# Performance work log

Hardware: AMD Instinct MI355X
Metric: run time of the kernel (lower is better)

## Reference

```python
import jax, jax.numpy as jnp
import numpy as np

NUM_HEADS = 16
D_MODEL = 1024
HEAD_DIM = D_MODEL // NUM_HEADS
SCALE = 8.0 / HEAD_DIM  # use_mup=True
LN_EPS = 1e-5


def setup_inputs() -> dict:
    key = jax.random.key(0)
    ks = jax.random.split(key, 8)
    B, N, M = 2, 2048, 2048
    std = 1.0 / np.sqrt(D_MODEL)
    return {
        "x1": jax.random.normal(ks[0], (B, N, D_MODEL), jnp.float32),
        "x2": jax.random.normal(ks[1], (B, M, D_MODEL), jnp.float32),
        "Wq": jax.random.normal(ks[2], (D_MODEL, D_MODEL), jnp.float32) * std,
        "Wk": jax.random.normal(ks[3], (D_MODEL, D_MODEL), jnp.float32) * std,
        "Wv": jax.random.normal(ks[4], (D_MODEL, D_MODEL), jnp.float32) * std,
        "Wp": jax.random.normal(ks[5], (D_MODEL, D_MODEL), jnp.float32) * std,
        "bp": jnp.zeros((D_MODEL,), jnp.float32),
        "ln_g": jnp.ones((HEAD_DIM,), jnp.float32),
        "ln_b": jnp.zeros((HEAD_DIM,), jnp.float32),
    }


def _layernorm(x, g, b):
    # LayerNorm over last dim (head_dim), eps=1e-5, biased variance (torch default)
    mu = jnp.mean(x, axis=-1, keepdims=True)
    var = jnp.mean(jnp.square(x - mu), axis=-1, keepdims=True)
    return (x - mu) * jax.lax.rsqrt(var + LN_EPS) * g + b


def reference(x1, x2, Wq, Wk, Wv, Wp, bp, ln_g, ln_b):
    B, N, C = x1.shape
    M = x2.shape[1]
    H, D = NUM_HEADS, HEAD_DIM
    # torch Linear: y = x @ W.T  (no qkv bias); reshape to [B, H, L, D]
    q = (x1 @ Wq.T).reshape(B, N, H, D).transpose(0, 2, 1, 3)
    k = (x2 @ Wk.T).reshape(B, M, H, D).transpose(0, 2, 1, 3)
    v = (x2 @ Wv.T).reshape(B, M, H, D).transpose(0, 2, 1, 3)
    # per-head QK LayerNorm (shared params)
    q = _layernorm(q, ln_g, ln_b)
    k = _layernorm(k, ln_g, ln_b)
    q = q * SCALE
    attn = jnp.einsum("bhnd,bhmd->bhnm", q, k)
    attn = jax.nn.softmax(attn, axis=-1)  # causal=False, attn_drop=0
    out = jnp.einsum("bhnm,bhmd->bhnd", attn, v)
    out = out.transpose(0, 2, 1, 3).reshape(B, N, C)
    return out @ Wp.T + bp
```

## Files before the change

kernel.cpp:

```cpp
#include <hip/hip_runtime.h>

#define DEV static __device__ __forceinline__

using bf16x8 = __attribute__((ext_vector_type(8))) short;
using f32x4  = __attribute__((ext_vector_type(4))) float;
using f32x16 = __attribute__((ext_vector_type(16))) float;

#if __has_builtin(__builtin_amdgcn_exp2f)
#define EXP2(x) __builtin_amdgcn_exp2f(x)
#else
#define EXP2(x) exp2f(x)
#endif

DEV unsigned short f2bf(float f) {
  union { float f; unsigned u; } v; v.f = f;
  return (unsigned short)((v.u + 0x7fffu + ((v.u >> 16) & 1u)) >> 16);
}
DEV float bf2f(unsigned short b) {
  union { unsigned u; float f; } v; v.u = ((unsigned)b) << 16;
  return v.f;
}
DEV unsigned cvtpk(float lo, float hi) {
  unsigned r;
  asm("v_cvt_pk_bf16_f32 %0, %1, %2" : "=v"(r) : "v"(lo), "v"(hi));
  return r;
}
DEV void pl32swap(unsigned &a, unsigned &b) {
  asm("v_permlane32_swap_b32 %0, %1" : "+v"(a), "+v"(b));
}
DEV bf16x8 mk8(unsigned a, unsigned b, unsigned c, unsigned d) {
  union { unsigned u[4]; bf16x8 v; } t;
  t.u[0] = a; t.u[1] = b; t.u[2] = c; t.u[3] = d;
  return t.v;
}
DEV f32x4 mfma16(bf16x8 a, bf16x8 b, f32x4 c) {
  return __builtin_amdgcn_mfma_f32_16x16x32_bf16(a, b, c, 0, 0, 0);
}
DEV f32x16 mfma32(bf16x8 a, bf16x8 b, f32x16 c) {
  return __builtin_amdgcn_mfma_f32_32x32x16_bf16(a, b, c, 0, 0, 0);
}
DEV f32x16 zero16() {
  f32x16 z;
#pragma unroll
  for (int i = 0; i < 16; ++i) z[i] = 0.f;
  return z;
}

typedef const __attribute__((address_space(1))) unsigned int* gas1;
typedef __attribute__((address_space(3))) unsigned int* las3;
DEV void gl16(const void* g, void* l) {
  __builtin_amdgcn_global_load_lds((gas1)g, (las3)l, 16, 0, 0);
}

__global__ __launch_bounds__(256, 8)
void conv_bf16(const float* __restrict__ x1, const float* __restrict__ x2,
               const float* __restrict__ Wq, const float* __restrict__ Wk,
               const float* __restrict__ Wv, const float* __restrict__ Wp,
               unsigned short* __restrict__ o)
{
  size_t e = ((size_t)blockIdx.x * 256 + threadIdx.x) * 8;
  const float* s; size_t off;
  if (e < 4194304u)       { s = x1; off = e; }
  else if (e < 8388608u)  { s = x2; off = e - 4194304u; }
  else if (e < 9437184u)  { s = Wq; off = e - 8388608u; }
  else if (e < 10485760u) { s = Wk; off = e - 9437184u; }
  else if (e < 11534336u) { s = Wv; off = e - 10485760u; }
  else                    { s = Wp; off = e - 11534336u; }
  const float4* p = reinterpret_cast<const float4*>(s + off);
  float4 a = p[0], b = p[1];
  int4 r;
  r.x = (int)cvtpk(a.x, a.y); r.y = (int)cvtpk(a.z, a.w);
  r.z = (int)cvtpk(b.x, b.y); r.w = (int)cvtpk(b.z, b.w);
  *reinterpret_cast<int4*>(o + e) = r;
}

__global__ __launch_bounds__(256, 2)
void gemm_qkv_bf(const unsigned short* __restrict__ xb,
                 const float* __restrict__ lg, const float* __restrict__ lb,
                 unsigned short* __restrict__ qb, unsigned short* __restrict__ kb,
                 unsigned short* __restrict__ vtb)
{
  __shared__ short As[128 * 64];
  __shared__ short Bs[128 * 64];
  const int tid = threadIdx.x;
  const int l = tid & 63, w = tid >> 6;
  const int wr = w >> 1, wc = w & 1;
  const int z = blockIdx.z;
  const unsigned short* A = (z == 0) ? xb : (xb + 4194304);
  const unsigned short* W = xb + 8388608 + (size_t)z * 1048576;
  const int id = blockIdx.x + (blockIdx.y << 3);
  const int tl = ((id & 7) << 5) | (id >> 3);
  const int bx = tl & 7, by = tl >> 3;
  const int brow = by * 128, bcol = bx * 128;

  const f32x4 zero = {0.f, 0.f, 0.f, 0.f};
  f32x4 acc[4][4];
#pragma unroll
  for (int mi = 0; mi < 4; ++mi)
#pragma unroll
    for (int ni = 0; ni < 4; ++ni) acc[mi][ni] = zero;

  const int srow = w * 32 + (l >> 3);
  const int scol = (l & 7) * 8;

  for (int kt = 0; kt < 16; ++kt) {
    const unsigned short* ga = A + (size_t)(brow + srow) * 1024 + kt * 64 + scol;
    const unsigned short* gb = W + (size_t)(bcol + srow) * 1024 + kt * 64 + scol;
#pragma unroll
    for (int i = 0; i < 4; ++i) {
      gl16(ga + (size_t)i * 8 * 1024, &As[(w * 32 + i * 8) * 64]);
      gl16(gb + (size_t)i * 8 * 1024, &Bs[(w * 32 + i * 8) * 64]);
    }
    __syncthreads();
#pragma unroll
    for (int kk = 0; kk < 2; ++kk) {
      const int k0 = kk * 32 + ((l >> 4) << 3);
      bf16x8 af[4], bfr[4];
#pragma unroll
      for (int mi = 0; mi < 4; ++mi)
        af[mi] = *reinterpret_cast<const bf16x8*>(
            &As[((wr << 6) + (mi << 4) + (l & 15)) * 64 + k0]);
#pragma unroll
      for (int ni = 0; ni < 4; ++ni)
        bfr[ni] = *reinterpret_cast<const bf16x8*>(
            &Bs[((wc << 6) + (ni << 4) + (l & 15)) * 64 + k0]);
#pragma unroll
      for (int mi = 0; mi < 4; ++mi)
#pragma unroll
        for (int ni = 0; ni < 4; ++ni)
          acc[mi][ni] = mfma16(af[mi], bfr[ni], acc[mi][ni]);
    }
    __syncthreads();
  }

  if (z < 2) {
    unsigned short* dst = (z == 0) ? qb : kb;
    const float scl = (z == 0) ? 0.18033688011112042f : 1.0f;
    const int h = bx * 2 + wc;
    float gw4[4], bw4[4];
#pragma unroll
    for (int ni = 0; ni < 4; ++ni) {
      gw4[ni] = lg[ni * 16 + (l & 15)] * scl;
      bw4[ni] = lb[ni * 16 + (l & 15)] * scl;
    }
#pragma unroll
    for (int mi = 0; mi < 4; ++mi) {
      float ylo[4];
#pragma unroll
      for (int r = 0; r < 4; ++r) {
        float v0 = acc[mi][0][r], v1 = acc[mi][1][r];
        float v2 = acc[mi][2][r], v3 = acc[mi][3][r];
        float s  = (v0 + v1) + (v2 + v3);
        float s2 = (v0 * v0 + v1 * v1) + (v2 * v2 + v3 * v3);
#pragma unroll
        for (int off = 1; off < 16; off <<= 1) {
          s  += __shfl_xor(s, off);
          s2 += __shfl_xor(s2, off);
        }
        float mean = s * (1.f / 64.f);
        float var  = s2 * (1.f / 64.f) - mean * mean;
        float rstd = rsqrtf(var + 1e-5f);
        float y[4];
        y[0] = (v0 - mean) * rstd * gw4[0] + bw4[0];
        y[1] = (v1 - mean) * rstd * gw4[1] + bw4[1];
        y[2] = (v2 - mean) * rstd * gw4[2] + bw4[2];
        y[3] = (v3 - mean) * rstd * gw4[3] + bw4[3];
        if (!(r & 1)) {
          ylo[0] = y[0]; ylo[1] = y[1]; ylo[2] = y[2]; ylo[3] = y[3];
        } else {
          int rowg0 = brow + (wr << 6) + (mi << 4) + ((l >> 4) << 2) + r - 1;
          int b = rowg0 >> 11, n = rowg0 & 2047;
          unsigned short* base =
              dst + (((size_t)(b * 16 + h) << 11) + n) * 64 + (l & 15);
#pragma unroll
          for (int ni = 0; ni < 4; ++ni) {
            unsigned u = cvtpk(ylo[ni], y[ni]);
            base[ni * 16]      = (unsigned short)(u & 0xffffu);
            base[ni * 16 + 64] = (unsigned short)(u >> 16);
          }
        }
      }
    }
  } else {
    const int bb = brow >> 11;
    const int nblk = brow & 2047;
#pragma unroll
    for (int mi = 0; mi < 4; ++mi)
#pragma unroll
      for (int ni = 0; ni < 4; ++ni) {
        int n0 = nblk + (wr << 6) + (mi << 4) + ((l >> 4) << 2);
        int colg = bcol + (wc << 6) + (ni << 4) + (l & 15);
        int h = colg >> 6, d = colg & 63;
        unsigned u0 = cvtpk(acc[mi][ni][0], acc[mi][ni][1]);
        unsigned u1 = cvtpk(acc[mi][ni][2], acc[mi][ni][3]);
        int2 u; u.x = (int)u0; u.y = (int)u1;
        *reinterpret_cast<int2*>(
            &vtb[((size_t)(bb * 16 + h) * 64 + d) * 2048 + n0]) = u;
      }
  }
}

__global__ __launch_bounds__(128)
void attn_fwd(const unsigned short* __restrict__ Q,
              const unsigned short* __restrict__ K,
              const unsigned short* __restrict__ Vt,
              unsigned short* __restrict__ pnum,
              float* __restrict__ plsum)
{
  __shared__ short Ks[2][64 * 64];
  __shared__ short Vs[2][64 * 64];
  const int tid = threadIdx.x, w = tid >> 6, l = tid & 63;
  const int lo5 = l & 31, hi = l >> 5;
  const int bh = blockIdx.y;
  const int half = blockIdx.z;
  const int tbase = half * 16;
  const int qbase = blockIdx.x * 64 + w * 32;
  const unsigned short* Qg = Q + ((size_t)bh * 2048 + qbase) * 64;
  const unsigned short* Kg = K + (size_t)bh * 2048 * 64;
  const unsigned short* Vg = Vt + (size_t)bh * 64 * 2048;

  bf16x8 qf[4];
#pragma unroll
  for (int ks = 0; ks < 4; ++ks)
    qf[ks] = *reinterpret_cast<const bf16x8*>(Qg + lo5 * 64 + ks * 16 + hi * 8);
  const bf16x8 ones = mk8(0x3F803F80u, 0x3F803F80u, 0x3F803F80u, 0x3F803F80u);

  f32x16 oc0 = zero16(), oc1 = zero16(), ls = zero16();

  const int srow = tid >> 3;
  const int sc8 = (tid & 7) * 8;
  const int swz = sc8 ^ ((srow & 7) << 3);

  int4 ka0, ka1, ka2, ka3, va0, va1, va2, va3;
  {
    const unsigned short* k0g = Kg + tbase * 4096;
    const unsigned short* v0g = Vg + tbase * 64;
    ka0 = *reinterpret_cast<const int4*>(k0g + (srow)      * 64 + sc8);
    ka1 = *reinterpret_cast<const int4*>(k0g + (srow + 16) * 64 + sc8);
    ka2 = *reinterpret_cast<const int4*>(k0g + (srow + 32) * 64 + sc8);
    ka3 = *reinterpret_cast<const int4*>(k0g + (srow + 48) * 64 + sc8);
    va0 = *reinterpret_cast<const int4*>(v0g + (size_t)(srow)      * 2048 + sc8);
    va1 = *reinterpret_cast<const int4*>(v0g + (size_t)(srow + 16) * 2048 + sc8);
    va2 = *reinterpret_cast<const int4*>(v0g + (size_t)(srow + 32) * 2048 + sc8);
    va3 = *reinterpret_cast<const int4*>(v0g + (size_t)(srow + 48) * 2048 + sc8);
  }
  *reinterpret_cast<int4*>(&Ks[0][((srow)      << 6) + swz]) = ka0;
  *reinterpret_cast<int4*>(&Ks[0][((srow + 16) << 6) + swz]) = ka1;
  *reinterpret_cast<int4*>(&Ks[0][((srow + 32) << 6) + swz]) = ka2;
  *reinterpret_cast<int4*>(&Ks[0][((srow + 48) << 6) + swz]) = ka3;
  *reinterpret_cast<int4*>(&Vs[0][((srow)      << 6) + swz]) = va0;
  *reinterpret_cast<int4*>(&Vs[0][((srow + 16) << 6) + swz]) = va1;
  *reinterpret_cast<int4*>(&Vs[0][((srow + 32) << 6) + swz]) = va2;
  *reinterpret_cast<int4*>(&Vs[0][((srow + 48) << 6) + swz]) = va3;
  __syncthreads();

  const unsigned short* kp = Kg + (tbase + 1) * 4096 + srow * 64 + sc8;
  const unsigned short* vp = Vg + (tbase + 1) * 64 + (size_t)srow * 2048 + sc8;

  for (int it = 0; it < 16; ++it) {
    const int cur = it & 1;
    const short* Kc = Ks[cur];
    const short* Vc = Vs[cur];

    if (it < 15) {
      ka0 = *reinterpret_cast<const int4*>(kp);
      ka1 = *reinterpret_cast<const int4*>(kp + 1024);
      ka2 = *reinterpret_cast<const int4*>(kp + 2048);
      ka3 = *reinterpret_cast<const int4*>(kp + 3072);
      va0 = *reinterpret_cast<const int4*>(vp);
      va1 = *reinterpret_cast<const int4*>(vp + 32768);
      va2 = *reinterpret_cast<const int4*>(vp + 65536);
      va3 = *reinterpret_cast<const int4*>(vp + 98304);
      kp += 4096; vp += 64;
    }

    f32x16 s0 = zero16(), s1 = zero16();
    __builtin_amdgcn_s_setprio(1);
#pragma unroll
    for (int ks = 0; ks < 4; ++ks) {
      const int colc = (16 * ks + 8 * hi) ^ ((lo5 & 7) << 3);
      bf16x8 k0 = *reinterpret_cast<const bf16x8*>(&Kc[(lo5 << 6) + colc]);
      s0 = mfma32(k0, qf[ks], s0);
      bf16x8 k1 = *reinterpret_cast<const bf16x8*>(&Kc[((32 + lo5) << 6) + colc]);
      s1 = mfma32(k1, qf[ks], s1);
    }
    __builtin_amdgcn_s_setprio(0);

    auto pvsub = [&](const f32x16& sv, int jbase) {
      float p0[16];
#pragma unroll
      for (int r = 0; r < 16; ++r) p0[r] = EXP2(sv[r]);
#pragma unroll
      for (int f = 0; f < 2; ++f) {
        unsigned x  = cvtpk(p0[8 * f + 0], p0[8 * f + 1]);
        unsigned zz = cvtpk(p0[8 * f + 2], p0[8 * f + 3]);
        unsigned y  = cvtpk(p0[8 * f + 4], p0[8 * f + 5]);
        unsigned ww = cvtpk(p0[8 * f + 6], p0[8 * f + 7]);
        pl32swap(x, y);
        pl32swap(zz, ww);
        bf16x8 pa = mk8(x, zz, y, ww);
        const int colc = (jbase + 16 * f + 8 * hi);
        bf16x8 v0 = *reinterpret_cast<const bf16x8*>(
            &Vc[(lo5 << 6) + (colc ^ ((lo5 & 7) << 3))]);
        bf16x8 v1 = *reinterpret_cast<const bf16x8*>(
            &Vc[((32 + lo5) << 6) + (colc ^ ((lo5 & 7) << 3))]);
        __builtin_amdgcn_s_setprio(1);
        oc0 = mfma32(pa, v0, oc0);
        oc1 = mfma32(pa, v1, oc1);
        ls  = mfma32(pa, ones, ls);
        __builtin_amdgcn_s_setprio(0);
      }
    };
    pvsub(s0, 0);
    pvsub(s1, 32);

    if (it < 15) {
      const int nb = cur ^ 1;
      *reinterpret_cast<int4*>(&Ks[nb][((srow)      << 6) + swz]) = ka0;
      *reinterpret_cast<int4*>(&Ks[nb][((srow + 16) << 6) + swz]) = ka1;
      *reinterpret_cast<int4*>(&Ks[nb][((srow + 32) << 6) + swz]) = ka2;
      *reinterpret_cast<int4*>(&Ks[nb][((srow + 48) << 6) + swz]) = ka3;
      *reinterpret_cast<int4*>(&Vs[nb][((srow)      << 6) + swz]) = va0;
      *reinterpret_cast<int4*>(&Vs[nb][((srow + 16) << 6) + swz]) = va1;
      *reinterpret_cast<int4*>(&Vs[nb][((srow + 32) << 6) + swz]) = va2;
      *reinterpret_cast<int4*>(&Vs[nb][((srow + 48) << 6) + swz]) = va3;
    }
    __syncthreads();
  }

  unsigned short* Pn = pnum + ((size_t)(half * 32 + bh) * 2048 + qbase) * 64;
#pragma unroll
  for (int r = 0; r < 16; ++r) {
    int qrow = (r & 3) + 8 * (r >> 2) + 4 * hi;
    Pn[qrow * 64 + lo5]      = f2bf(oc0[r]);
    Pn[qrow * 64 + 32 + lo5] = f2bf(oc1[r]);
  }
  if (lo5 == 0) {
    float* Pl = plsum + (size_t)(half * 32 + bh) * 2048 + qbase;
#pragma unroll
    for (int r = 0; r < 16; ++r)
      Pl[(r & 3) + 8 * (r >> 2) + 4 * hi] = ls[r];
  }
}

__global__ __launch_bounds__(256, 8)
void attn_combine(const unsigned short* __restrict__ pnum,
                  const float* __restrict__ plsum,
                  unsigned short* __restrict__ obuf)
{
  const int t = blockIdx.x * 256 + threadIdx.x;
  const int bh = t >> 14;
  const int rem = t & 16383;
  const int q = rem >> 3, dblk = rem & 7;
  const size_t i0 = (((size_t)bh * 2048) + q) * 64 + dblk * 8;
  const size_t i1 = i0 + (size_t)32 * 2048 * 64;
  ushort4 a0 = *reinterpret_cast<const ushort4*>(pnum + i0);
  ushort4 a1 = *reinterpret_cast<const ushort4*>(pnum + i0 + 4);
  ushort4 b0 = *reinterpret_cast<const ushort4*>(pnum + i1);
  ushort4 b1 = *reinterpret_cast<const ushort4*>(pnum + i1 + 4);
  float ls = plsum[bh * 2048 + q] + plsum[65536 + bh * 2048 + q];
  float inv = 1.f / ls;
  ushort4 o0, o1;
  o0.x = f2bf((bf2f(a0.x) + bf2f(b0.x)) * inv);
  o0.y = f2bf((bf2f(a0.y) + bf2f(b0.y)) * inv);
  o0.z = f2bf((bf2f(a0.z) + bf2f(b0.z)) * inv);
  o0.w = f2bf((bf2f(a0.w) + bf2f(b0.w)) * inv);
  o1.x = f2bf((bf2f(a1.x) + bf2f(b1.x)) * inv);
  o1.y = f2bf((bf2f(a1.y) + bf2f(b1.y)) * inv);
  o1.z = f2bf((bf2f(a1.z) + bf2f(b1.z)) * inv);
  o1.w = f2bf((bf2f(a1.w) + bf2f(b1.w)) * inv);
  unsigned short* dst = obuf + ((size_t)(bh >> 4) * 2048 + q) * 1024 +
                        (bh & 15) * 64 + dblk * 8;
  *reinterpret_cast<ushort4*>(dst) = o0;
  *reinterpret_cast<ushort4*>(dst + 4) = o1;
}

__global__ __launch_bounds__(256, 2)
void gemm_out_bf(const unsigned short* __restrict__ ob,
                 const unsigned short* __restrict__ wpb,
                 const float* __restrict__ bp, float* __restrict__ out)
{
  __shared__ short As[128 * 64];
  __shared__ short Bs[128 * 64];
  const int tid = threadIdx.x;
  const int l = tid & 63, w = tid >> 6;
  const int wr = w >> 1, wc = w & 1;
  const int id = blockIdx.x + (blockIdx.y << 3);
  const int tl = ((id & 7) << 5) | (id >> 3);
  const int brow = (tl >> 3) * 128, bcol = (tl & 7) * 128;

  const f32x4 zero = {0.f, 0.f, 0.f, 0.f};
  f32x4 acc[4][4];
#pragma unroll
  for (int mi = 0; mi < 4; ++mi)
#pragma unroll
    for (int ni = 0; ni < 4; ++ni) acc[mi][ni] = zero;

  const int srow = w * 32 + (l >> 3);
  const int scol = (l & 7) * 8;

  for (int kt = 0; kt < 16; ++kt) {
    const unsigned short* ga = ob + (size_t)(brow + srow) * 1024 + kt * 64 + scol;
    const unsigned short* gb = wpb + (size_t)(bcol + srow) * 1024 + kt * 64 + scol;
#pragma unroll
    for (int i = 0; i < 4; ++i) {
      gl16(ga + (size_t)i * 8 * 1024, &As[(w * 32 + i * 8) * 64]);
      gl16(gb + (size_t)i * 8 * 1024, &Bs[(w * 32 + i * 8) * 64]);
    }
    __syncthreads();
#pragma unroll
    for (int kk = 0; kk < 2; ++kk) {
      const int k0 = kk * 32 + ((l >> 4) << 3);
      bf16x8 af[4], bfr[4];
#pragma unroll
      for (int mi = 0; mi < 4; ++mi)
        af[mi] = *reinterpret_cast<const bf16x8*>(
            &As[((wr << 6) + (mi << 4) + (l & 15)) * 64 + k0]);
#pragma unroll
      for (int ni = 0; ni < 4; ++ni)
        bfr[ni] = *reinterpret_cast<const bf16x8*>(
            &Bs[((wc << 6) + (ni << 4) + (l & 15)) * 64 + k0]);
#pragma unroll
      for (int mi = 0; mi < 4; ++mi)
#pragma unroll
        for (int ni = 0; ni < 4; ++ni)
          acc[mi][ni] = mfma16(af[mi], bfr[ni], acc[mi][ni]);
    }
    __syncthreads();
  }

  float bias[4];
#pragma unroll
  for (int ni = 0; ni < 4; ++ni)
    bias[ni] = bp[bcol + (wc << 6) + (ni << 4) + (l & 15)];
#pragma unroll
  for (int mi = 0; mi < 4; ++mi)
#pragma unroll
    for (int ni = 0; ni < 4; ++ni)
#pragma unroll
      for (int r = 0; r < 4; ++r) {
        int rowg = brow + (wr << 6) + (mi << 4) + ((l >> 4) << 2) + r;
        int colg = bcol + (wc << 6) + (ni << 4) + (l & 15);
        out[(size_t)rowg * 1024 + colg] = acc[mi][ni][r] + bias[ni];
      }
}

extern "C" void kernel_launch(void* const* d_in, const int* in_sizes, int n_in,
                              void* d_out, int out_size, void* d_ws, size_t ws_size,
                              hipStream_t stream)
{
  const float* x1 = (const float*)d_in[0];
  const float* x2 = (const float*)d_in[1];
  const float* Wq = (const float*)d_in[2];
  const float* Wk = (const float*)d_in[3];
  const float* Wv = (const float*)d_in[4];
  const float* Wp = (const float*)d_in[5];
  const float* bp = (const float*)d_in[6];
  const float* lg = (const float*)d_in[7];
  const float* lb = (const float*)d_in[8];

  char* wsb = (char*)d_ws;
  unsigned short* xb   = (unsigned short*)wsb;
  unsigned short* qb   = (unsigned short*)(wsb + 25165824);
  unsigned short* kb   = qb + 4194304;
  unsigned short* vtb  = kb + 4194304;
  unsigned short* obuf = vtb + 4194304;
  unsigned short* pnum = obuf + 4194304;
  float* plsum = (float*)(wsb + 75497472);
  float* out = (float*)d_out;

  conv_bf16<<<6144, 256, 0, stream>>>(x1, x2, Wq, Wk, Wv, Wp, xb);
  gemm_qkv_bf<<<dim3(8, 32, 3), 256, 0, stream>>>(xb, lg, lb, qb, kb, vtb);
  attn_fwd<<<dim3(32, 32, 2), 128, 0, stream>>>(qb, kb, vtb, pnum, plsum);
  attn_combine<<<2048, 256, 0, stream>>>(pnum, plsum, obuf);
  gemm_out_bf<<<dim3(8, 32), 256, 0, stream>>>(obuf,
      xb + 11534336, bp, out);
}
```

Baseline: 143.1 us.

## Process two 32-row query tiles per wave to reuse K/V LDS fragments

Result: faster. 127.0 us (-11.3%).

```diff
diff --git a/kernel.cpp b/kernel.cpp
--- a/kernel.cpp
+++ b/kernel.cpp
@@ -200,7 +200,7 @@
   }
 }
 
-__global__ __launch_bounds__(128)
+__global__ __launch_bounds__(128, 2)
 void attn_fwd(const unsigned short* __restrict__ Q,
               const unsigned short* __restrict__ K,
               const unsigned short* __restrict__ Vt,
@@ -214,18 +214,21 @@
   const int bh = blockIdx.y;
   const int half = blockIdx.z;
   const int tbase = half * 16;
-  const int qbase = blockIdx.x * 64 + w * 32;
+  const int qbase = blockIdx.x * 128 + w * 64;
   const unsigned short* Qg = Q + ((size_t)bh * 2048 + qbase) * 64;
   const unsigned short* Kg = K + (size_t)bh * 2048 * 64;
   const unsigned short* Vg = Vt + (size_t)bh * 64 * 2048;
 
-  bf16x8 qf[4];
-#pragma unroll
-  for (int ks = 0; ks < 4; ++ks)
-    qf[ks] = *reinterpret_cast<const bf16x8*>(Qg + lo5 * 64 + ks * 16 + hi * 8);
+  bf16x8 qfA[4], qfB[4];
+#pragma unroll
+  for (int ks = 0; ks < 4; ++ks) {
+    qfA[ks] = *reinterpret_cast<const bf16x8*>(Qg + lo5 * 64 + ks * 16 + hi * 8);
+    qfB[ks] = *reinterpret_cast<const bf16x8*>(Qg + (32 + lo5) * 64 + ks * 16 + hi * 8);
+  }
   const bf16x8 ones = mk8(0x3F803F80u, 0x3F803F80u, 0x3F803F80u, 0x3F803F80u);
 
-  f32x16 oc0 = zero16(), oc1 = zero16(), ls = zero16();
+  f32x16 oc0a = zero16(), oc1a = zero16(), lsa = zero16();
+  f32x16 oc0b = zero16(), oc1b = zero16(), lsb = zero16();
 
   const int srow = tid >> 3;
   const int sc8 = (tid & 7) * 8;
@@ -274,45 +277,57 @@
       kp += 4096; vp += 64;
     }
 
-    f32x16 s0 = zero16(), s1 = zero16();
+    f32x16 s0a = zero16(), s1a = zero16(), s0b = zero16(), s1b = zero16();
     __builtin_amdgcn_s_setprio(1);
 #pragma unroll
     for (int ks = 0; ks < 4; ++ks) {
       const int colc = (16 * ks + 8 * hi) ^ ((lo5 & 7) << 3);
       bf16x8 k0 = *reinterpret_cast<const bf16x8*>(&Kc[(lo5 << 6) + colc]);
-      s0 = mfma32(k0, qf[ks], s0);
       bf16x8 k1 = *reinterpret_cast<const bf16x8*>(&Kc[((32 + lo5) << 6) + colc]);
-      s1 = mfma32(k1, qf[ks], s1);
+      s0a = mfma32(k0, qfA[ks], s0a);
+      s1a = mfma32(k1, qfA[ks], s1a);
+      s0b = mfma32(k0, qfB[ks], s0b);
+      s1b = mfma32(k1, qfB[ks], s1b);
     }
     __builtin_amdgcn_s_setprio(0);
 
-    auto pvsub = [&](const f32x16& sv, int jbase) {
-      float p0[16];
-#pragma unroll
-      for (int r = 0; r < 16; ++r) p0[r] = EXP2(sv[r]);
+    auto pvpair = [&](const f32x16& sa, const f32x16& sb, int jbase) {
+      float pA[16], pB[16];
+#pragma unroll
+      for (int r = 0; r < 16; ++r) { pA[r] = EXP2(sa[r]); pB[r] = EXP2(sb[r]); }
 #pragma unroll
       for (int f = 0; f < 2; ++f) {
-        unsigned x  = cvtpk(p0[8 * f + 0], p0[8 * f + 1]);
-        unsigned zz = cvtpk(p0[8 * f + 2], p0[8 * f + 3]);
-        unsigned y  = cvtpk(p0[8 * f + 4], p0[8 * f + 5]);
-        unsigned ww = cvtpk(p0[8 * f + 6], p0[8 * f + 7]);
-        pl32swap(x, y);
-        pl32swap(zz, ww);
-        bf16x8 pa = mk8(x, zz, y, ww);
+        unsigned xA  = cvtpk(pA[8 * f + 0], pA[8 * f + 1]);
+        unsigned zA  = cvtpk(pA[8 * f + 2], pA[8 * f + 3]);
+        unsigned yA  = cvtpk(pA[8 * f + 4], pA[8 * f + 5]);
+        unsigned wA  = cvtpk(pA[8 * f + 6], pA[8 * f + 7]);
+        pl32swap(xA, yA);
+        pl32swap(zA, wA);
+        bf16x8 paA = mk8(xA, zA, yA, wA);
+        unsigned xB  = cvtpk(pB[8 * f + 0], pB[8 * f + 1]);
+        unsigned zB  = cvtpk(pB[8 * f + 2], pB[8 * f + 3]);
+        unsigned yB  = cvtpk(pB[8 * f + 4], pB[8 * f + 5]);
+        unsigned wB  = cvtpk(pB[8 * f + 6], pB[8 * f + 7]);
+        pl32swap(xB, yB);
+        pl32swap(zB, wB);
+        bf16x8 paB = mk8(xB, zB, yB, wB);
         const int colc = (jbase + 16 * f + 8 * hi);
         bf16x8 v0 = *reinterpret_cast<const bf16x8*>(
             &Vc[(lo5 << 6) + (colc ^ ((lo5 & 7) << 3))]);
         bf16x8 v1 = *reinterpret_cast<const bf16x8*>(
             &Vc[((32 + lo5) << 6) + (colc ^ ((lo5 & 7) << 3))]);
         __builtin_amdgcn_s_setprio(1);
-        oc0 = mfma32(pa, v0, oc0);
-        oc1 = mfma32(pa, v1, oc1);
-        ls  = mfma32(pa, ones, ls);
+        oc0a = mfma32(paA, v0, oc0a);
+        oc1a = mfma32(paA, v1, oc1a);
+        lsa  = mfma32(paA, ones, lsa);
+        oc0b = mfma32(paB, v0, oc0b);
+        oc1b = mfma32(paB, v1, oc1b);
+        lsb  = mfma32(paB, ones, lsb);
         __builtin_amdgcn_s_setprio(0);
       }
     };
-    pvsub(s0, 0);
-    pvsub(s1, 32);
+    pvpair(s0a, s0b, 0);
+    pvpair(s1a, s1b, 32);
 
     if (it < 15) {
       const int nb = cur ^ 1;
@@ -332,14 +347,19 @@
 #pragma unroll
   for (int r = 0; r < 16; ++r) {
     int qrow = (r & 3) + 8 * (r >> 2) + 4 * hi;
-    Pn[qrow * 64 + lo5]      = f2bf(oc0[r]);
-    Pn[qrow * 64 + 32 + lo5] = f2bf(oc1[r]);
+    Pn[qrow * 64 + lo5]             = f2bf(oc0a[r]);
+    Pn[qrow * 64 + 32 + lo5]        = f2bf(oc1a[r]);
+    Pn[(32 + qrow) * 64 + lo5]      = f2bf(oc0b[r]);
+    Pn[(32 + qrow) * 64 + 32 + lo5] = f2bf(oc1b[r]);
   }
   if (lo5 == 0) {
     float* Pl = plsum + (size_t)(half * 32 + bh) * 2048 + qbase;
 #pragma unroll
-    for (int r = 0; r < 16; ++r)
-      Pl[(r & 3) + 8 * (r >> 2) + 4 * hi] = ls[r];
+    for (int r = 0; r < 16; ++r) {
+      int qrow = (r & 3) + 8 * (r >> 2) + 4 * hi;
+      Pl[qrow]      = lsa[r];
+      Pl[32 + qrow] = lsb[r];
+    }
   }
 }
 
@@ -471,7 +491,7 @@
 
   conv_bf16<<<6144, 256, 0, stream>>>(x1, x2, Wq, Wk, Wv, Wp, xb);
   gemm_qkv_bf<<<dim3(8, 32, 3), 256, 0, stream>>>(xb, lg, lb, qb, kb, vtb);
-  attn_fwd<<<dim3(32, 32, 2), 128, 0, stream>>>(qb, kb, vtb, pnum, plsum);
+  attn_fwd<<<dim3(16, 32, 2), 128, 0, stream>>>(qb, kb, vtb, pnum, plsum);
   attn_combine<<<2048, 256, 0, stream>>>(pnum, plsum, obuf);
   gemm_out_bf<<<dim3(8, 32), 256, 0, stream>>>(obuf,
       xb + 11534336, bp, out);
```
